# Optimization experiments

Hardware: AMD Instinct MI355X
Metric: run time of the kernel (lower is better)

## Reference

```python
import jax, jax.numpy as jnp
import numpy as np

V, EMB, ENC, DEC = 50000, 256, 512, 512
E2 = ENC * 2            # bidirectional encoder output dim = 1024
B, S1, S2 = 128, 200, 200
NEG = -1e10


def _bahdanau(hidden, enc_out, mask, W, b, v):
    # hidden [B,DEC], enc_out [S,B,E2], mask [B,S] -> weights [B,S]
    S = enc_out.shape[0]
    h = jnp.broadcast_to(hidden[None], (S,) + hidden.shape)          # [S,B,DEC]
    energy = jnp.tanh(jnp.concatenate([h, enc_out], axis=-1) @ W + b)  # [S,B,DEC]
    scores = energy @ v                                              # [S,B]
    scores = jnp.where(mask.T == 0, NEG, scores)
    return jax.nn.softmax(scores, axis=0).T                          # [B,S]


def setup_inputs() -> dict:
    key = jax.random.key(0)
    ks = jax.random.split(key, 20)
    f = lambda k, shp, s=0.05: jax.random.normal(k, shp, dtype=jnp.float32) * s
    inp = {
        "input": jax.random.randint(ks[0], (B,), 0, V),
        "hidden": f(ks[1], (B, DEC), 1.0),
        "src1": jax.random.randint(ks[2], (S1, B), 0, V),
        "encoder_outputs1": f(ks[3], (S1, B, E2), 1.0),
        "mask1": jnp.ones((B, S1), dtype=jnp.int32),
        "triple_mask": jnp.ones((B, S1), dtype=jnp.int32),
        "encoder_outputs2": f(ks[4], (S2, B, E2), 1.0),
        "mask2": jnp.ones((B, S2), dtype=jnp.int32),
        # parameters
        "embedding": f(ks[5], (V, EMB)),
        "attn_W": f(ks[6], (E2 + DEC, DEC)),
        "attn_b": jnp.zeros((DEC,), jnp.float32),
        "attn_v": f(ks[7], (DEC,)),
        "copy_W": f(ks[8], (E2 + DEC, DEC)),
        "copy_b": jnp.zeros((DEC,), jnp.float32),
        "copy_v": f(ks[9], (DEC,)),
        "gru_Wih": f(ks[10], (3 * DEC, E2 + EMB)),
        "gru_Whh": f(ks[11], (3 * DEC, DEC)),
        "gru_bih": jnp.zeros((3 * DEC,), jnp.float32),
        "gru_bhh": jnp.zeros((3 * DEC,), jnp.float32),
        "fc_W": f(ks[12], (V, E2 + DEC)),
        "fc_b": jnp.zeros((V,), jnp.float32),
        "gate_W": f(ks[13], (1, E2 + EMB)),
        "gate_b": jnp.zeros((1,), jnp.float32),
    }
    return inp


def reference(input, hidden, src1, encoder_outputs1, mask1, triple_mask,
              encoder_outputs2, mask2, embedding, attn_W, attn_b, attn_v,
              copy_W, copy_b, copy_v, gru_Wih, gru_Whh, gru_bih, gru_bhh,
              fc_W, fc_b, gate_W, gate_b):
    # embed current token (dropout = identity at eval)
    emb = embedding[input]                                           # [B,EMB]
    # joint attention over concatenated encoders
    enc = jnp.concatenate([encoder_outputs1, encoder_outputs2], axis=0)  # [S1+S2,B,E2]
    mask = jnp.concatenate([mask1, mask2], axis=1)                   # [B,S1+S2]
    a = _bahdanau(hidden, enc, mask, attn_W, attn_b, attn_v)         # [B,S1+S2]
    weighted = jnp.einsum('bs,sbe->be', a, enc)                      # [B,E2]
    # single-step GRU (PyTorch gate layout: r, z, n)
    x = jnp.concatenate([emb, weighted], axis=-1)                    # [B,E2+EMB]
    gx = x @ gru_Wih.T + gru_bih
    gh = hidden @ gru_Whh.T + gru_bhh
    xr, xz, xn = jnp.split(gx, 3, axis=-1)
    hr, hz, hn = jnp.split(gh, 3, axis=-1)
    r = jax.nn.sigmoid(xr + hr)
    z = jax.nn.sigmoid(xz + hz)
    n = jnp.tanh(xn + r * hn)
    h_new = (1.0 - z) * n + z * hidden                               # [B,DEC]
    # generation distribution
    state = jnp.concatenate([h_new, weighted], axis=1)               # [B,DEC+E2]
    vocab_dist = jax.nn.softmax(state @ fc_W.T + fc_b, axis=-1)      # [B,V]
    # copy gate + copy attention over encoder 1 only
    p_gen = jax.nn.sigmoid(jnp.concatenate([weighted, emb], axis=-1) @ gate_W.T + gate_b)  # [B,1]
    attn_dist = _bahdanau(h_new, encoder_outputs1, mask1 * triple_mask,
                          copy_W, copy_b, copy_v)                    # [B,S1]
    vd = p_gen * vocab_dist
    ad = (1.0 - p_gen) * attn_dist
    # scatter_add copy probabilities into vocab slots
    b_idx = jnp.arange(vd.shape[0])[:, None]                         # [B,1]
    final_dist = vd.at[b_idx, src1.T].add(ad)                        # [B,V]
    return final_dist, h_new
```

## Files before the change

kernel.cpp:

```cpp
#include <hip/hip_runtime.h>
#include <math.h>

#define BB   128
#define DECD 512
#define E2D  1024
#define EMBD 256
#define S1D  200
#define S2D  200
#define SJD  400
#define VV   50000
#define NEGV (-1e10f)
#define JY   800

typedef unsigned short u16;
typedef __bf16 bf16x8 __attribute__((ext_vector_type(8)));
typedef float f32x4 __attribute__((ext_vector_type(4)));
typedef u16 u16x8 __attribute__((ext_vector_type(8)));

__device__ __forceinline__ u16 f2bf(float x) {
  unsigned u = __float_as_uint(x);
  unsigned r = (u + 0x7fffu + ((u >> 16) & 1u)) >> 16;
  return (u16)r;
}
__device__ __forceinline__ float bf2f(u16 h) {
  return __uint_as_float(((unsigned)h) << 16);
}
__device__ __forceinline__ u16x8 cvt8h(float4 a, float4 b) {
  bf16x8 r;
  r[0] = (__bf16)a.x; r[1] = (__bf16)a.y; r[2] = (__bf16)a.z; r[3] = (__bf16)a.w;
  r[4] = (__bf16)b.x; r[5] = (__bf16)b.y; r[6] = (__bf16)b.z; r[7] = (__bf16)b.w;
  return *reinterpret_cast<u16x8*>(&r);
}

typedef const __attribute__((address_space(1))) void* gas_t;
typedef __attribute__((address_space(3))) void* las_t;
__device__ __forceinline__ void async_copy16(const u16* g, u16* l) {
  __builtin_amdgcn_global_load_lds((gas_t)g, (las_t)l, 16, 0, 0);
}

__global__ __launch_bounds__(256) void k_prep(
    const float* __restrict__ Wa, const float* __restrict__ Wc,
    u16* __restrict__ Wta, u16* __restrict__ Wtc,
    const float* __restrict__ hidden, u16* __restrict__ hid_bf,
    const float* __restrict__ attn_b, float* __restrict__ hWa,
    const int* __restrict__ inp, const float* __restrict__ table,
    u16* __restrict__ x_bf) {
  int blk = blockIdx.x, tid = threadIdx.x;
  if (blk < 1024) {
    __shared__ float t[32][33];
    int z = blk >> 9, rem = blk & 511;
    int bk = rem & 31, bn = rem >> 5;
    const float* W = z ? Wc : Wa;
    u16* Wt = z ? Wtc : Wta;
    int tx = tid & 31, ty = tid >> 5;
    #pragma unroll
    for (int r = 0; r < 4; ++r) {
      int k = bk * 32 + ty + r * 8;
      t[ty + r * 8][tx] = W[(size_t)(512 + k) * 512 + bn * 32 + tx];
    }
    __syncthreads();
    #pragma unroll
    for (int r = 0; r < 4; ++r) {
      int n = bn * 32 + ty + r * 8;
      Wt[(size_t)n * 1024 + bk * 32 + tx] = f2bf(t[tx][ty + r * 8]);
    }
  } else if (blk < 1056) {
    int i = (blk - 1024) * 256 + tid;
    const float4 f0 = *(const float4*)(hidden + (size_t)i * 8);
    const float4 f1 = *(const float4*)(hidden + (size_t)i * 8 + 4);
    *(u16x8*)(hid_bf + (size_t)i * 8) = cvt8h(f0, f1);
  } else if (blk < 1312) {
    int idx = blk - 1056;
    int b = idx >> 1;
    int d = (idx & 1) * 256 + tid;
    const float* hr = hidden + (size_t)b * DECD;
    float acc = attn_b[d];
    #pragma unroll 8
    for (int k = 0; k < DECD; ++k) acc += hr[k] * Wa[(size_t)k * DECD + d];
    hWa[(size_t)b * DECD + d] = acc;
  } else {
    int b = blk - 1312;
    x_bf[(size_t)b * 1280 + tid] = f2bf(table[(size_t)inp[b] * EMBD + tid]);
  }
}

__global__ __launch_bounds__(256) void gemm_energy_jc(
    const float* __restrict__ enc1, const float* __restrict__ enc2,
    const u16* __restrict__ BtA, const u16* __restrict__ BtC,
    const float* __restrict__ hW, const float* __restrict__ v,
    float* __restrict__ partJ, float* __restrict__ preC) {
  __shared__ u16 As[2][64 * 32];
  __shared__ u16 Bs[256 * 32];
  __shared__ float sbuf[64][2];
  int tid = threadIdx.x;
  int wid = tid >> 6, lane = tid & 63;
  int wr = wid >> 1, wc = wid & 1;
  int bn = blockIdx.x;
  int jy = blockIdx.y;
  int joint = (jy < JY);
  size_t m0 = joint ? (size_t)jy * 64 : (size_t)(jy - JY) * 64;
  int bhalf = (jy & 1) * 64;
  int n0 = bn * 256;

  int rA = tid >> 2, cslot = tid & 3;
  int lAoff = rA * 32 + ((cslot ^ ((rA >> 1) & 3)) * 8);
  const float* base;
  if (joint)
    base = (m0 < (size_t)S1D * BB) ? (enc1 + m0 * E2D)
                                   : (enc2 + (m0 - (size_t)S1D * BB) * E2D);
  else
    base = enc1 + m0 * E2D;
  const float* gA_f = base + (size_t)rA * E2D + cslot * 8;

  const u16* Bt = joint ? BtA : BtC;
  const u16* gB[4];
  #pragma unroll
  for (int i = 0; i < 4; ++i) {
    int rn = i * 64 + wid * 16 + (lane >> 2);
    int c = (lane & 3) ^ ((rn >> 1) & 3);
    gB[i] = Bt + (size_t)(n0 + rn) * E2D + c * 8;
  }

  int q = lane >> 4, cl = lane & 15;
  int aoff[2], boff[8];
  #pragma unroll
  for (int mi = 0; mi < 2; ++mi) {
    int row = wr * 32 + mi * 16 + cl;
    aoff[mi] = row * 64 + ((q ^ ((row >> 1) & 3)) * 16);
  }
  #pragma unroll
  for (int nj = 0; nj < 8; ++nj) {
    int rn = wc * 128 + nj * 16 + cl;
    boff[nj] = rn * 64 + ((q ^ ((rn >> 1) & 3)) * 16);
  }

  f32x4 acc[2][8];
  #pragma unroll
  for (int mi = 0; mi < 2; ++mi)
    #pragma unroll
    for (int nj = 0; nj < 8; ++nj) {
      f32x4 z = {0.f, 0.f, 0.f, 0.f};
      acc[mi][nj] = z;
    }

  float4 a0 = *(const float4*)(gA_f);
  float4 a1 = *(const float4*)(gA_f + 4);
  *(u16x8*)(&As[0][lAoff]) = cvt8h(a0, a1);
  a0 = *(const float4*)(gA_f + 32);
  a1 = *(const float4*)(gA_f + 36);

  for (int t = 0; t < 32; ++t) {
    int cur = t & 1, nxt = cur ^ 1;
    int k0 = t * 32, k1 = k0 + 32;
    #pragma unroll
    for (int i = 0; i < 4; ++i) async_copy16(gB[i] + k0, &Bs[2048 * i + wid * 512]);
    if (t < 31) {
      *(u16x8*)(&As[nxt][lAoff]) = cvt8h(a0, a1);
      if (t < 30) {
        a0 = *(const float4*)(gA_f + k1 + 32);
        a1 = *(const float4*)(gA_f + k1 + 36);
      }
    }
    __syncthreads();
    bf16x8 af[2];
    #pragma unroll
    for (int mi = 0; mi < 2; ++mi)
      af[mi] = *(const bf16x8*)((const char*)As[cur] + aoff[mi]);
    #pragma unroll
    for (int nj = 0; nj < 8; ++nj) {
      bf16x8 bg = *(const bf16x8*)((const char*)Bs + boff[nj]);
      acc[0][nj] = __builtin_amdgcn_mfma_f32_16x16x32_bf16(af[0], bg, acc[0][nj], 0, 0, 0);
      acc[1][nj] = __builtin_amdgcn_mfma_f32_16x16x32_bf16(af[1], bg, acc[1][nj], 0, 0, 0);
    }
    __syncthreads();
  }

  if (joint) {
    #pragma unroll
    for (int mi = 0; mi < 2; ++mi) {
      #pragma unroll
      for (int j = 0; j < 4; ++j) {
        int m = wr * 32 + mi * 16 + q * 4 + j;
        float s = 0.f;
        #pragma unroll
        for (int nj = 0; nj < 8; ++nj) {
          int d = n0 + wc * 128 + nj * 16 + cl;
          s += tanhf(acc[mi][nj][j] + hW[(size_t)(bhalf + m) * DECD + d]) * v[d];
        }
        s += __shfl_xor(s, 1, 64);
        s += __shfl_xor(s, 2, 64);
        s += __shfl_xor(s, 4, 64);
        s += __shfl_xor(s, 8, 64);
        if (cl == 0) sbuf[m][wc] = s;
      }
    }
    __syncthreads();
    if (tid < 64)
      partJ[(size_t)bn * 51200 + m0 + tid] = sbuf[tid][0] + sbuf[tid][1];
  } else {
    #pragma unroll
    for (int mi = 0; mi < 2; ++mi) {
      #pragma unroll
      for (int nj = 0; nj < 8; ++nj) {
        int d = n0 + wc * 128 + nj * 16 + cl;
        #pragma unroll
        for (int j = 0; j < 4; ++j) {
          int m = wr * 32 + mi * 16 + q * 4 + j;
          preC[(m0 + m) * (size_t)DECD + d] = acc[mi][nj][j];
        }
      }
    }
  }
}

__global__ __launch_bounds__(256) void k_copy_epi(const float* __restrict__ preC,
    const float* __restrict__ hWc, const float* __restrict__ v,
    float* __restrict__ scC) {
  int r = blockIdx.x * 4 + (threadIdx.x >> 6);
  int lane = threadIdx.x & 63;
  int b = r & 127, s = r >> 7;
  const float* pr = preC + (size_t)r * DECD + lane * 8;
  const float* hr = hWc + (size_t)b * DECD + lane * 8;
  const float* vr = v + lane * 8;
  float4 p0 = *(const float4*)(pr),     p1 = *(const float4*)(pr + 4);
  float4 h0 = *(const float4*)(hr),     h1 = *(const float4*)(hr + 4);
  float4 v0 = *(const float4*)(vr),     v1 = *(const float4*)(vr + 4);
  float acc = tanhf(p0.x + h0.x) * v0.x + tanhf(p0.y + h0.y) * v0.y
            + tanhf(p0.z + h0.z) * v0.z + tanhf(p0.w + h0.w) * v0.w
            + tanhf(p1.x + h1.x) * v1.x + tanhf(p1.y + h1.y) * v1.y
            + tanhf(p1.z + h1.z) * v1.z + tanhf(p1.w + h1.w) * v1.w;
  #pragma unroll
  for (int off = 32; off > 0; off >>= 1) acc += __shfl_xor(acc, off, 64);
  if (lane == 0) scC[(size_t)b * S1D + s] = acc;
}

__global__ __launch_bounds__(256) void k_wpart_sm(const float* __restrict__ part,
    const float* __restrict__ enc1, const float* __restrict__ enc2,
    const int* __restrict__ m1, const int* __restrict__ m2,
    float* __restrict__ wp) {
  int b = blockIdx.x, tid = threadIdx.x;
  int e2 = blockIdx.y * 256 + tid;
  int scn = blockIdx.z;
  __shared__ float sm[4];
  __shared__ float ws[100];
  int s0 = tid, s2 = tid + 256;
  float a0, a1 = -INFINITY;
  {
    int msk = (s0 < S1D) ? m1[b * S1D + s0] : m2[b * S2D + (s0 - S1D)];
    int m = s0 * 128 + b;
    a0 = msk ? (part[m] + part[51200 + m]) : NEGV;
  }
  if (s2 < SJD) {
    int msk = (s2 < S1D) ? m1[b * S1D + s2] : m2[b * S2D + (s2 - S1D)];
    int m = s2 * 128 + b;
    a1 = msk ? (part[m] + part[51200 + m]) : NEGV;
  }
  float vmax = fmaxf(a0, a1);
  #pragma unroll
  for (int off = 32; off > 0; off >>= 1) vmax = fmaxf(vmax, __shfl_down(vmax, off, 64));
  int lane = tid & 63, wid = tid >> 6;
  if (lane == 0) sm[wid] = vmax;
  __syncthreads();
  vmax = fmaxf(fmaxf(sm[0], sm[1]), fmaxf(sm[2], sm[3]));
  __syncthreads();
  float lsum = expf(a0 - vmax);
  if (s2 < SJD) lsum += expf(a1 - vmax);
  #pragma unroll
  for (int off = 32; off > 0; off >>= 1) lsum += __shfl_down(lsum, off, 64);
  if (lane == 0) sm[wid] = lsum;
  __syncthreads();
  float inv = 1.0f / (sm[0] + sm[1] + sm[2] + sm[3]);
  if (tid < 100) {
    int s = scn * 100 + tid;
    int msk = (s < S1D) ? m1[b * S1D + s] : m2[b * S2D + (s - S1D)];
    int m = s * 128 + b;
    float av = msk ? (part[m] + part[51200 + m]) : NEGV;
    ws[tid] = expf(av - vmax) * inv;
  }
  __syncthreads();
  float acc0 = 0.f, acc1 = 0.f;
  #pragma unroll 4
  for (int i = 0; i < 100; ++i) {
    int s = scn * 100 + i;
    const float* ep = (s < S1D) ? (enc1 + ((size_t)s * BB + b) * E2D)
                                : (enc2 + ((size_t)(s - S1D) * BB + b) * E2D);
    float2 u = *(const float2*)(ep + e2 * 2);
    float w = ws[i];
    acc0 += w * u.x;
    acc1 += w * u.y;
  }
  float* dst = wp + ((size_t)scn * BB + b) * E2D + e2 * 2;
  dst[0] = acc0;
  dst[1] = acc1;
}

__global__ __launch_bounds__(256) void k_wsum_x(const float* __restrict__ wp,
    float* __restrict__ wgt, u16* __restrict__ x) {
  int i = blockIdx.x * 256 + threadIdx.x;
  const int NN = BB * E2D;
  float s = wp[i] + wp[NN + i] + wp[2 * NN + i] + wp[3 * NN + i];
  wgt[i] = s;
  int b = i >> 10, e = i & 1023;
  x[(size_t)b * 1280 + EMBD + e] = f2bf(s);
}

__device__ __forceinline__ void fc2_body(
    const u16* __restrict__ A, const float* __restrict__ Bf,
    const float* __restrict__ bias, float* __restrict__ C,
    int N, int K, int n0) {
  __shared__ u16 As[2][128 * 32];
  __shared__ u16 Bs[2][128 * 32];
  int tid = threadIdx.x;
  int wid = tid >> 6, lane = tid & 63;
  int wr = wid >> 2, wc = wid & 3;

  int rowa = wid * 16 + (lane >> 2);
  int ca = (lane & 3) ^ ((rowa >> 1) & 3);
  const u16* gA = A + (size_t)rowa * K + ca * 8;

  int rB = tid >> 2, cB = tid & 3;
  int gnB = n0 + rB; if (gnB >= N) gnB = N - 1;
  const float* gB = Bf + (size_t)gnB * K + cB * 8;
  int lBoff = rB * 32 + ((cB ^ ((rB >> 1) & 3)) * 8);

  int q = lane >> 4, cl = lane & 15;
  int aoff[4], boff[2];
  #pragma unroll
  for (int mi = 0; mi < 4; ++mi) {
    int row = wr * 64 + mi * 16 + cl;
    aoff[mi] = row * 64 + ((q ^ ((row >> 1) & 3)) * 16);
  }
  #pragma unroll
  for (int nj = 0; nj < 2; ++nj) {
    int rn = wc * 32 + nj * 16 + cl;
    boff[nj] = rn * 64 + ((q ^ ((rn >> 1) & 3)) * 16);
  }

  f32x4 acc[4][2];
  #pragma unroll
  for (int mi = 0; mi < 4; ++mi)
    #pragma unroll
    for (int nj = 0; nj < 2; ++nj) {
      f32x4 z = {0.f, 0.f, 0.f, 0.f};
      acc[mi][nj] = z;
    }

  for (int k0 = 0; k0 < K; k0 += 64) {
    float4 b00 = *(const float4*)(gB + k0);
    float4 b01 = *(const float4*)(gB + k0 + 4);
    float4 b10 = *(const float4*)(gB + k0 + 32);
    float4 b11 = *(const float4*)(gB + k0 + 36);
    *(u16x8*)(&Bs[0][lBoff]) = cvt8h(b00, b01);
    *(u16x8*)(&Bs[1][lBoff]) = cvt8h(b10, b11);
    async_copy16(gA + k0,      &As[0][wid * 512]);
    async_copy16(gA + k0 + 32, &As[1][wid * 512]);
    __syncthreads();
    #pragma unroll
    for (int h = 0; h < 2; ++h) {
      bf16x8 af[4], bg[2];
      #pragma unroll
      for (int mi = 0; mi < 4; ++mi) af[mi] = *(const bf16x8*)((const char*)As[h] + aoff[mi]);
      #pragma unroll
      for (int nj = 0; nj < 2; ++nj) bg[nj] = *(const bf16x8*)((const char*)Bs[h] + boff[nj]);
      #pragma unroll
      for (int mi = 0; mi < 4; ++mi)
        #pragma unroll
        for (int nj = 0; nj < 2; ++nj)
          acc[mi][nj] = __builtin_amdgcn_mfma_f32_16x16x32_bf16(af[mi], bg[nj], acc[mi][nj], 0, 0, 0);
    }
    __syncthreads();
  }

  #pragma unroll
  for (int mi = 0; mi < 4; ++mi) {
    #pragma unroll
    for (int nj = 0; nj < 2; ++nj) {
      int n = n0 + wc * 32 + nj * 16 + cl;
      if (n < N) {
        float bv = bias[n];
        #pragma unroll
        for (int j = 0; j < 4; ++j) {
          int m = wr * 64 + mi * 16 + q * 4 + j;
          C[(size_t)m * N + n] = acc[mi][nj][j] + bv;
        }
      }
    }
  }
}

__global__ __launch_bounds__(512) void gemm_gru(
    const u16* __restrict__ x_bf, const float* __restrict__ Wih,
    const float* __restrict__ bih, float* __restrict__ gx,
    const u16* __restrict__ h_bf, const float* __restrict__ Whh,
    const float* __restrict__ bhh, float* __restrict__ gh) {
  if (blockIdx.x < 12)
    fc2_body(x_bf, Wih, bih, gx, 1536, 1280, blockIdx.x * 128);
  else
    fc2_body(h_bf, Whh, bhh, gh, 1536, 512, (blockIdx.x - 12) * 128);
}

__global__ __launch_bounds__(512) void gemm_fc3(
    const u16* __restrict__ A, const float* __restrict__ Bf,
    const float* __restrict__ bias, float* __restrict__ C,
    int N, int K) {
  __shared__ u16 As[2][128 * 32];
  __shared__ u16 Bs[2][64 * 32];
  int tid = threadIdx.x;
  int wid = tid >> 6, lane = tid & 63;
  int wr = wid >> 2, wc = wid & 3;
  int n0 = blockIdx.x * 64;

  int rowa = wid * 16 + (lane >> 2);
  int ca = (lane & 3) ^ ((rowa >> 1) & 3);
  const u16* gA = A + (size_t)rowa * K + ca * 8;

  int rB = tid >> 3, cB = tid & 7;
  int gnB = n0 + rB; if (gnB >= N) gnB = N - 1;
  const float* gB = Bf + (size_t)gnB * K + cB * 8;
  int hB = cB >> 2, s4 = cB & 3;
  int lBoff = rB * 32 + ((s4 ^ ((rB >> 1) & 3)) * 8);

  int q = lane >> 4, cl = lane & 15;
  int aoff[4], boff;
  #pragma unroll
  for (int mi = 0; mi < 4; ++mi) {
    int row = wr * 64 + mi * 16 + cl;
    aoff[mi] = row * 64 + ((q ^ ((row >> 1) & 3)) * 16);
  }
  {
    int rn = wc * 16 + cl;
    boff = rn * 64 + ((q ^ ((rn >> 1) & 3)) * 16);
  }

  f32x4 acc[4];
  #pragma unroll
  for (int mi = 0; mi < 4; ++mi) {
    f32x4 z = {0.f, 0.f, 0.f, 0.f};
    acc[mi] = z;
  }

  float4 b0 = *(const float4*)(gB);
  float4 b1 = *(const float4*)(gB + 4);

  for (int k0 = 0; k0 < K; k0 += 64) {
    *(u16x8*)(&Bs[hB][lBoff]) = cvt8h(b0, b1);
    async_copy16(gA + k0,      &As[0][wid * 512]);
    async_copy16(gA + k0 + 32, &As[1][wid * 512]);
    __syncthreads();
    if (k0 + 64 < K) {
      b0 = *(const float4*)(gB + k0 + 64);
      b1 = *(const float4*)(gB + k0 + 68);
    }
    #pragma unroll
    for (int h = 0; h < 2; ++h) {
      bf16x8 af[4];
      #pragma unroll
      for (int mi = 0; mi < 4; ++mi) af[mi] = *(const bf16x8*)((const char*)As[h] + aoff[mi]);
      bf16x8 bg = *(const bf16x8*)((const char*)Bs[h] + boff);
      #pragma unroll
      for (int mi = 0; mi < 4; ++mi)
        acc[mi] = __builtin_amdgcn_mfma_f32_16x16x32_bf16(af[mi], bg, acc[mi], 0, 0, 0);
    }
    __syncthreads();
  }

  int n = n0 + wc * 16 + cl;
  if (n < N) {
    float bv = bias[n];
    #pragma unroll
    for (int mi = 0; mi < 4; ++mi)
      #pragma unroll
      for (int j = 0; j < 4; ++j) {
        int m = wr * 64 + mi * 16 + q * 4 + j;
        C[(size_t)m * N + n] = acc[mi][j] + bv;
      }
  }
}

__global__ __launch_bounds__(256) void k_gru_concat(const float* __restrict__ gx,
    const float* __restrict__ gh, const float* __restrict__ hidden,
    const float* __restrict__ wgt, float* __restrict__ hnew,
    u16* __restrict__ st) {
  int b = blockIdx.x, tid = threadIdx.x;
  #pragma unroll
  for (int qq = 0; qq < 2; ++qq) {
    int d = tid + qq * 256;
    size_t o = (size_t)b * 1536;
    float xr = gx[o + d],        hr = gh[o + d];
    float xz = gx[o + 512 + d],  hz = gh[o + 512 + d];
    float xn = gx[o + 1024 + d], hn = gh[o + 1024 + d];
    float r = 1.f / (1.f + expf(-(xr + hr)));
    float z = 1.f / (1.f + expf(-(xz + hz)));
    float n = tanhf(xn + r * hn);
    float hv = (1.f - z) * n + z * hidden[(size_t)b * DECD + d];
    hnew[(size_t)b * DECD + d] = hv;
    st[(size_t)b * 1536 + d] = f2bf(hv);
  }
  #pragma unroll
  for (int qq = 0; qq < 4; ++qq) {
    int e = tid + qq * 256;
    st[(size_t)b * 1536 + DECD + e] = f2bf(wgt[(size_t)b * E2D + e]);
  }
}

__global__ __launch_bounds__(256) void k_pgen_partial(const float* __restrict__ wgt,
    const int* __restrict__ inp, const float* __restrict__ table,
    const float* __restrict__ gW, const float* __restrict__ gb,
    float* __restrict__ pg,
    const float* __restrict__ hnew, const float* __restrict__ copy_W,
    const float* __restrict__ copy_b, float* __restrict__ hWc) {
  int tid = threadIdx.x;
  if (blockIdx.x < 128) {
    int b = blockIdx.x;
    __shared__ float sm[4];
    float s = 0.f;
    for (int k = tid; k < E2D + EMBD; k += 256)
      s += gW[k] * ((k < E2D) ? wgt[(size_t)b * E2D + k]
                              : table[(size_t)inp[b] * EMBD + k - E2D]);
    #pragma unroll
    for (int off = 32; off > 0; off >>= 1) s += __shfl_down(s, off, 64);
    int lane = tid & 63, wid = tid >> 6;
    if (lane == 0) sm[wid] = s;
    __syncthreads();
    if (tid == 0) {
      float t = sm[0] + sm[1] + sm[2] + sm[3] + gb[0];
      pg[b] = 1.f / (1.f + expf(-t));
    }
  } else {
    int idx = blockIdx.x - 128;
    int b = idx >> 1;
    int d = (idx & 1) * 256 + tid;
    const float* hr = hnew + (size_t)b * DECD;
    float acc = copy_b[d];
    #pragma unroll 8
    for (int k = 0; k < DECD; ++k) acc += hr[k] * copy_W[(size_t)k * DECD + d];
    hWc[(size_t)b * DECD + d] = acc;
  }
}

__global__ __launch_bounds__(256) void k_vocab_sc2(float* __restrict__ dist,
    const float* __restrict__ pg, const float* __restrict__ scC,
    const int* __restrict__ m1, const int* __restrict__ tr,
    const int* __restrict__ src1) {
  int b = blockIdx.x, tid = threadIdx.x;
  float* row = dist + (size_t)b * VV;
  __shared__ float sm[4];
  int lane = tid & 63, wid = tid >> 6;
  float m = -INFINITY;
  for (int i = tid; i < VV; i += 256) m = fmaxf(m, row[i]);
  #pragma unroll
  for (int off = 32; off > 0; off >>= 1) m = fmaxf(m, __shfl_down(m, off, 64));
  if (lane == 0) sm[wid] = m;
  __syncthreads();
  m = fmaxf(fmaxf(sm[0], sm[1]), fmaxf(sm[2], sm[3]));
  __syncthreads();
  float s = 0.f;
  for (int i = tid; i < VV; i += 256) s += expf(row[i] - m);
  #pragma unroll
  for (int off = 32; off > 0; off >>= 1) s += __shfl_down(s, off, 64);
  if (lane == 0) sm[wid] = s;
  __syncthreads();
  s = sm[0] + sm[1] + sm[2] + sm[3];
  float pgb = pg[b];
  float scale = pgb / s;
  for (int i = tid; i < VV; i += 256) row[i] = expf(row[i] - m) * scale;
  __syncthreads();
  float c0 = -INFINITY;
  if (tid < S1D) {
    int msk = m1[b * S1D + tid] * tr[b * S1D + tid];
    c0 = msk ? scC[(size_t)b * S1D + tid] : NEGV;
  }
  float cmax = c0;
  #pragma unroll
  for (int off = 32; off > 0; off >>= 1) cmax = fmaxf(cmax, __shfl_down(cmax, off, 64));
  if (lane == 0) sm[wid] = cmax;
  __syncthreads();
  cmax = fmaxf(fmaxf(sm[0], sm[1]), fmaxf(sm[2], sm[3]));
  __syncthreads();
  float csum = (tid < S1D) ? expf(c0 - cmax) : 0.f;
  #pragma unroll
  for (int off = 32; off > 0; off >>= 1) csum += __shfl_down(csum, off, 64);
  if (lane == 0) sm[wid] = csum;
  __syncthreads();
  float cinv = 1.0f / (sm[0] + sm[1] + sm[2] + sm[3]);
  if (tid < S1D) {
    float val = (1.f - pgb) * expf(c0 - cmax) * cinv;
    int tok = src1[(size_t)tid * BB + b];
    atomicAdd(&row[tok], val);
  }
}

extern "C" void kernel_launch(void* const* d_in, const int* in_sizes, int n_in,
                              void* d_out, int out_size, void* d_ws, size_t ws_size,
                              hipStream_t stream) {
  (void)in_sizes; (void)n_in; (void)out_size; (void)ws_size;
  const int*   input  = (const int*)d_in[0];
  const float* hidden = (const float*)d_in[1];
  const int*   src1   = (const int*)d_in[2];
  const float* enc1   = (const float*)d_in[3];
  const int*   mask1  = (const int*)d_in[4];
  const int*   triple = (const int*)d_in[5];
  const float* enc2   = (const float*)d_in[6];
  const int*   mask2  = (const int*)d_in[7];
  const float* embedding = (const float*)d_in[8];
  const float* attn_W = (const float*)d_in[9];
  const float* attn_b = (const float*)d_in[10];
  const float* attn_v = (const float*)d_in[11];
  const float* copy_W = (const float*)d_in[12];
  const float* copy_b = (const float*)d_in[13];
  const float* copy_v = (const float*)d_in[14];
  const float* gru_Wih = (const float*)d_in[15];
  const float* gru_Whh = (const float*)d_in[16];
  const float* gru_bih = (const float*)d_in[17];
  const float* gru_bhh = (const float*)d_in[18];
  const float* fc_W   = (const float*)d_in[19];
  const float* fc_b   = (const float*)d_in[20];
  const float* gate_W = (const float*)d_in[21];
  const float* gate_b = (const float*)d_in[22];

  char* w = (char*)d_ws;
  u16* Wt_a = (u16*)w;                w += (size_t)512 * 1024 * 2;
  u16* Wt_c = (u16*)w;                w += (size_t)512 * 1024 * 2;
  float* partJ = (float*)w;           w += (size_t)2 * 51200 * 4;
  float* preC = (float*)w;            w += (size_t)25600 * 512 * 4;
  float* hWa  = (float*)w;            w += (size_t)BB * DECD * 4;
  float* hWc  = (float*)w;            w += (size_t)BB * DECD * 4;
  float* scC  = (float*)w;            w += (size_t)BB * S1D * 4;
  float* wgt  = (float*)w;            w += (size_t)BB * E2D * 4;
  float* wpart = (float*)w;           w += (size_t)4 * BB * E2D * 4;
  u16*   x_bf = (u16*)w;              w += (size_t)BB * 1280 * 2;
  u16*   hid_bf = (u16*)w;            w += (size_t)BB * DECD * 2;
  float* gx   = (float*)w;            w += (size_t)BB * 1536 * 4;
  float* gh   = (float*)w;            w += (size_t)BB * 1536 * 4;
  u16*   st_bf = (u16*)w;             w += (size_t)BB * 1536 * 2;
  float* pg   = (float*)w;            w += 512;

  float* out  = (float*)d_out;
  float* hnew = out + (size_t)BB * VV;

  k_prep<<<1440, 256, 0, stream>>>(attn_W, copy_W, Wt_a, Wt_c,
                                   hidden, hid_bf, attn_b, hWa,
                                   input, embedding, x_bf);

  gemm_energy_jc<<<dim3(2, JY + 400), 256, 0, stream>>>(
      enc1, enc2, Wt_a, Wt_c, hWa, attn_v, partJ, preC);

  k_wpart_sm<<<dim3(BB, 2, 4), 256, 0, stream>>>(partJ, enc1, enc2, mask1, mask2, wpart);
  k_wsum_x<<<512, 256, 0, stream>>>(wpart, wgt, x_bf);

  gemm_gru<<<24, 512, 0, stream>>>(x_bf, gru_Wih, gru_bih, gx,
                                   hid_bf, gru_Whh, gru_bhh, gh);
  k_gru_concat<<<BB, 256, 0, stream>>>(gx, gh, hidden, wgt, hnew, st_bf);

  gemm_fc3<<<(VV + 63) / 64, 512, 0, stream>>>(st_bf, fc_W, fc_b, out, VV, 1536);

  k_pgen_partial<<<384, 256, 0, stream>>>(wgt, input, embedding, gate_W, gate_b, pg,
                                          hnew, copy_W, copy_b, hWc);
  k_copy_epi<<<25600 / 4, 256, 0, stream>>>(preC, hWc, copy_v, scC);

  k_vocab_sc2<<<BB, 256, 0, stream>>>(out, pg, scC, mask1, triple, src1);
}
```

Baseline: 576.6 us.

## Fuse p_gen, copy-hidden projection and copy scores into the fc GEMM launch

New measurement: 565.5 us. No clear change (-1.9%).

```diff
diff --git a/kernel.cpp b/kernel.cpp
--- a/kernel.cpp
+++ b/kernel.cpp
@@ -213,27 +213,6 @@
   }
 }
 
-__global__ __launch_bounds__(256) void k_copy_epi(const float* __restrict__ preC,
-    const float* __restrict__ hWc, const float* __restrict__ v,
-    float* __restrict__ scC) {
-  int r = blockIdx.x * 4 + (threadIdx.x >> 6);
-  int lane = threadIdx.x & 63;
-  int b = r & 127, s = r >> 7;
-  const float* pr = preC + (size_t)r * DECD + lane * 8;
-  const float* hr = hWc + (size_t)b * DECD + lane * 8;
-  const float* vr = v + lane * 8;
-  float4 p0 = *(const float4*)(pr),     p1 = *(const float4*)(pr + 4);
-  float4 h0 = *(const float4*)(hr),     h1 = *(const float4*)(hr + 4);
-  float4 v0 = *(const float4*)(vr),     v1 = *(const float4*)(vr + 4);
-  float acc = tanhf(p0.x + h0.x) * v0.x + tanhf(p0.y + h0.y) * v0.y
-            + tanhf(p0.z + h0.z) * v0.z + tanhf(p0.w + h0.w) * v0.w
-            + tanhf(p1.x + h1.x) * v1.x + tanhf(p1.y + h1.y) * v1.y
-            + tanhf(p1.z + h1.z) * v1.z + tanhf(p1.w + h1.w) * v1.w;
-  #pragma unroll
-  for (int off = 32; off > 0; off >>= 1) acc += __shfl_xor(acc, off, 64);
-  if (lane == 0) scC[(size_t)b * S1D + s] = acc;
-}
-
 __global__ __launch_bounds__(256) void k_wpart_sm(const float* __restrict__ part,
     const float* __restrict__ enc1, const float* __restrict__ enc2,
     const int* __restrict__ m1, const int* __restrict__ m2,
@@ -399,81 +378,137 @@
     fc2_body(h_bf, Whh, bhh, gh, 1536, 512, (blockIdx.x - 12) * 128);
 }
 
-__global__ __launch_bounds__(512) void gemm_fc3(
+__global__ __launch_bounds__(512) void gemm_fc3c(
     const u16* __restrict__ A, const float* __restrict__ Bf,
-    const float* __restrict__ bias, float* __restrict__ C,
-    int N, int K) {
-  __shared__ u16 As[2][128 * 32];
-  __shared__ u16 Bs[2][64 * 32];
+    const float* __restrict__ bias, float* __restrict__ C, int N, int K,
+    const float* __restrict__ wgt, const int* __restrict__ inp,
+    const float* __restrict__ table, const float* __restrict__ gW,
+    const float* __restrict__ gb, float* __restrict__ pg,
+    const float* __restrict__ hnew, const float* __restrict__ copy_W,
+    const float* __restrict__ copy_b, const float* __restrict__ copy_v,
+    const float* __restrict__ preC, float* __restrict__ scC) {
+  __shared__ u16 smem[12288];
   int tid = threadIdx.x;
-  int wid = tid >> 6, lane = tid & 63;
-  int wr = wid >> 2, wc = wid & 3;
-  int n0 = blockIdx.x * 64;
-
-  int rowa = wid * 16 + (lane >> 2);
-  int ca = (lane & 3) ^ ((rowa >> 1) & 3);
-  const u16* gA = A + (size_t)rowa * K + ca * 8;
-
-  int rB = tid >> 3, cB = tid & 7;
-  int gnB = n0 + rB; if (gnB >= N) gnB = N - 1;
-  const float* gB = Bf + (size_t)gnB * K + cB * 8;
-  int hB = cB >> 2, s4 = cB & 3;
-  int lBoff = rB * 32 + ((s4 ^ ((rB >> 1) & 3)) * 8);
-
-  int q = lane >> 4, cl = lane & 15;
-  int aoff[4], boff;
-  #pragma unroll
-  for (int mi = 0; mi < 4; ++mi) {
-    int row = wr * 64 + mi * 16 + cl;
-    aoff[mi] = row * 64 + ((q ^ ((row >> 1) & 3)) * 16);
-  }
-  {
-    int rn = wc * 16 + cl;
-    boff = rn * 64 + ((q ^ ((rn >> 1) & 3)) * 16);
-  }
-
-  f32x4 acc[4];
-  #pragma unroll
-  for (int mi = 0; mi < 4; ++mi) {
-    f32x4 z = {0.f, 0.f, 0.f, 0.f};
-    acc[mi] = z;
-  }
-
-  float4 b0 = *(const float4*)(gB);
-  float4 b1 = *(const float4*)(gB + 4);
-
-  for (int k0 = 0; k0 < K; k0 += 64) {
-    *(u16x8*)(&Bs[hB][lBoff]) = cvt8h(b0, b1);
-    async_copy16(gA + k0,      &As[0][wid * 512]);
-    async_copy16(gA + k0 + 32, &As[1][wid * 512]);
-    __syncthreads();
-    if (k0 + 64 < K) {
-      b0 = *(const float4*)(gB + k0 + 64);
-      b1 = *(const float4*)(gB + k0 + 68);
-    }
-    #pragma unroll
-    for (int h = 0; h < 2; ++h) {
-      bf16x8 af[4];
-      #pragma unroll
-      for (int mi = 0; mi < 4; ++mi) af[mi] = *(const bf16x8*)((const char*)As[h] + aoff[mi]);
-      bf16x8 bg = *(const bf16x8*)((const char*)Bs[h] + boff);
+  if (blockIdx.x < 782) {
+    u16* As0 = smem;            u16* As1 = smem + 4096;
+    u16* Bs0 = smem + 8192;     u16* Bs1 = smem + 10240;
+    u16* AsH[2] = {As0, As1};
+    u16* BsH[2] = {Bs0, Bs1};
+    int wid = tid >> 6, lane = tid & 63;
+    int wr = wid >> 2, wc = wid & 3;
+    int n0 = blockIdx.x * 64;
+
+    int rowa = wid * 16 + (lane >> 2);
+    int ca = (lane & 3) ^ ((rowa >> 1) & 3);
+    const u16* gA = A + (size_t)rowa * K + ca * 8;
+
+    int rB = tid >> 3, cB = tid & 7;
+    int gnB = n0 + rB; if (gnB >= N) gnB = N - 1;
+    const float* gB = Bf + (size_t)gnB * K + cB * 8;
+    int hB = cB >> 2, s4 = cB & 3;
+    int lBoff = rB * 32 + ((s4 ^ ((rB >> 1) & 3)) * 8);
+
+    int q = lane >> 4, cl = lane & 15;
+    int aoff[4], boff;
+    #pragma unroll
+    for (int mi = 0; mi < 4; ++mi) {
+      int row = wr * 64 + mi * 16 + cl;
+      aoff[mi] = row * 64 + ((q ^ ((row >> 1) & 3)) * 16);
+    }
+    {
+      int rn = wc * 16 + cl;
+      boff = rn * 64 + ((q ^ ((rn >> 1) & 3)) * 16);
+    }
+
+    f32x4 acc[4];
+    #pragma unroll
+    for (int mi = 0; mi < 4; ++mi) {
+      f32x4 z = {0.f, 0.f, 0.f, 0.f};
+      acc[mi] = z;
+    }
+
+    float4 b0 = *(const float4*)(gB);
+    float4 b1 = *(const float4*)(gB + 4);
+
+    for (int k0 = 0; k0 < K; k0 += 64) {
+      *(u16x8*)(&BsH[hB][lBoff]) = cvt8h(b0, b1);
+      async_copy16(gA + k0,      &As0[wid * 512]);
+      async_copy16(gA + k0 + 32, &As1[wid * 512]);
+      __syncthreads();
+      if (k0 + 64 < K) {
+        b0 = *(const float4*)(gB + k0 + 64);
+        b1 = *(const float4*)(gB + k0 + 68);
+      }
+      #pragma unroll
+      for (int h = 0; h < 2; ++h) {
+        bf16x8 af[4];
+        #pragma unroll
+        for (int mi = 0; mi < 4; ++mi) af[mi] = *(const bf16x8*)((const char*)AsH[h] + aoff[mi]);
+        bf16x8 bg = *(const bf16x8*)((const char*)BsH[h] + boff);
+        #pragma unroll
+        for (int mi = 0; mi < 4; ++mi)
+          acc[mi] = __builtin_amdgcn_mfma_f32_16x16x32_bf16(af[mi], bg, acc[mi], 0, 0, 0);
+      }
+      __syncthreads();
+    }
+
+    int n = n0 + wc * 16 + cl;
+    if (n < N) {
+      float bv = bias[n];
       #pragma unroll
       for (int mi = 0; mi < 4; ++mi)
-        acc[mi] = __builtin_amdgcn_mfma_f32_16x16x32_bf16(af[mi], bg, acc[mi], 0, 0, 0);
-    }
-    __syncthreads();
-  }
-
-  int n = n0 + wc * 16 + cl;
-  if (n < N) {
-    float bv = bias[n];
-    #pragma unroll
-    for (int mi = 0; mi < 4; ++mi)
-      #pragma unroll
-      for (int j = 0; j < 4; ++j) {
-        int m = wr * 64 + mi * 16 + q * 4 + j;
-        C[(size_t)m * N + n] = acc[mi][j] + bv;
-      }
+        #pragma unroll
+        for (int j = 0; j < 4; ++j) {
+          int m = wr * 64 + mi * 16 + q * 4 + j;
+          C[(size_t)m * N + n] = acc[mi][j] + bv;
+        }
+    }
+  } else if (blockIdx.x < 910) {
+    int b = blockIdx.x - 782;
+    float* sm = (float*)smem;
+    float s = 0.f;
+    for (int k = tid; k < E2D + EMBD; k += 512)
+      s += gW[k] * ((k < E2D) ? wgt[(size_t)b * E2D + k]
+                              : table[(size_t)inp[b] * EMBD + k - E2D]);
+    #pragma unroll
+    for (int off = 32; off > 0; off >>= 1) s += __shfl_down(s, off, 64);
+    int lane = tid & 63, wid = tid >> 6;
+    if (lane == 0) sm[wid] = s;
+    __syncthreads();
+    if (tid == 0) {
+      float t = sm[0] + sm[1] + sm[2] + sm[3] + sm[4] + sm[5] + sm[6] + sm[7] + gb[0];
+      pg[b] = 1.f / (1.f + expf(-t));
+    }
+  } else {
+    int b = blockIdx.x - 910;
+    float* hn  = (float*)smem;
+    float* hwc = (float*)smem + 512;
+    hn[tid] = hnew[(size_t)b * DECD + tid];
+    __syncthreads();
+    {
+      float acc = copy_b[tid];
+      #pragma unroll 8
+      for (int k = 0; k < DECD; ++k) acc += hn[k] * copy_W[(size_t)k * DECD + tid];
+      hwc[tid] = acc;
+    }
+    __syncthreads();
+    int wid = tid >> 6, lane = tid & 63;
+    float4 h0 = *(const float4*)(hwc + lane * 8);
+    float4 h1 = *(const float4*)(hwc + lane * 8 + 4);
+    float4 v0 = *(const float4*)(copy_v + lane * 8);
+    float4 v1 = *(const float4*)(copy_v + lane * 8 + 4);
+    for (int s = wid; s < S1D; s += 8) {
+      const float* pr = preC + ((size_t)s * 128 + b) * DECD + lane * 8;
+      float4 p0 = *(const float4*)(pr);
+      float4 p1 = *(const float4*)(pr + 4);
+      float e = tanhf(p0.x + h0.x) * v0.x + tanhf(p0.y + h0.y) * v0.y
+              + tanhf(p0.z + h0.z) * v0.z + tanhf(p0.w + h0.w) * v0.w
+              + tanhf(p1.x + h1.x) * v1.x + tanhf(p1.y + h1.y) * v1.y
+              + tanhf(p1.z + h1.z) * v1.z + tanhf(p1.w + h1.w) * v1.w;
+      #pragma unroll
+      for (int off = 32; off > 0; off >>= 1) e += __shfl_xor(e, off, 64);
+      if (lane == 0) scC[(size_t)b * S1D + s] = e;
+    }
   }
 }
 
@@ -500,41 +535,6 @@
   for (int qq = 0; qq < 4; ++qq) {
     int e = tid + qq * 256;
     st[(size_t)b * 1536 + DECD + e] = f2bf(wgt[(size_t)b * E2D + e]);
-  }
-}
-
-__global__ __launch_bounds__(256) void k_pgen_partial(const float* __restrict__ wgt,
-    const int* __restrict__ inp, const float* __restrict__ table,
-    const float* __restrict__ gW, const float* __restrict__ gb,
-    float* __restrict__ pg,
-    const float* __restrict__ hnew, const float* __restrict__ copy_W,
-    const float* __restrict__ copy_b, float* __restrict__ hWc) {
-  int tid = threadIdx.x;
-  if (blockIdx.x < 128) {
-    int b = blockIdx.x;
-    __shared__ float sm[4];
-    float s = 0.f;
-    for (int k = tid; k < E2D + EMBD; k += 256)
-      s += gW[k] * ((k < E2D) ? wgt[(size_t)b * E2D + k]
-                              : table[(size_t)inp[b] * EMBD + k - E2D]);
-    #pragma unroll
-    for (int off = 32; off > 0; off >>= 1) s += __shfl_down(s, off, 64);
-    int lane = tid & 63, wid = tid >> 6;
-    if (lane == 0) sm[wid] = s;
-    __syncthreads();
-    if (tid == 0) {
-      float t = sm[0] + sm[1] + sm[2] + sm[3] + gb[0];
-      pg[b] = 1.f / (1.f + expf(-t));
-    }
-  } else {
-    int idx = blockIdx.x - 128;
-    int b = idx >> 1;
-    int d = (idx & 1) * 256 + tid;
-    const float* hr = hnew + (size_t)b * DECD;
-    float acc = copy_b[d];
-    #pragma unroll 8
-    for (int k = 0; k < DECD; ++k) acc += hr[k] * copy_W[(size_t)k * DECD + d];
-    hWc[(size_t)b * DECD + d] = acc;
   }
 }
 
@@ -624,7 +624,6 @@
   float* partJ = (float*)w;           w += (size_t)2 * 51200 * 4;
   float* preC = (float*)w;            w += (size_t)25600 * 512 * 4;
   float* hWa  = (float*)w;            w += (size_t)BB * DECD * 4;
-  float* hWc  = (float*)w;            w += (size_t)BB * DECD * 4;
   float* scC  = (float*)w;            w += (size_t)BB * S1D * 4;
   float* wgt  = (float*)w;            w += (size_t)BB * E2D * 4;
   float* wpart = (float*)w;           w += (size_t)4 * BB * E2D * 4;
@@ -652,11 +651,10 @@
                                    hid_bf, gru_Whh, gru_bhh, gh);
   k_gru_concat<<<BB, 256, 0, stream>>>(gx, gh, hidden, wgt, hnew, st_bf);
 
-  gemm_fc3<<<(VV + 63) / 64, 512, 0, stream>>>(st_bf, fc_W, fc_b, out, VV, 1536);
-
-  k_pgen_partial<<<384, 256, 0, stream>>>(wgt, input, embedding, gate_W, gate_b, pg,
-                                          hnew, copy_W, copy_b, hWc);
-  k_copy_epi<<<25600 / 4, 256, 0, stream>>>(preC, hWc, copy_v, scC);
+  gemm_fc3c<<<782 + 128 + 128, 512, 0, stream>>>(
+      st_bf, fc_W, fc_b, out, VV, 1536,
+      wgt, input, embedding, gate_W, gate_b, pg,
+      hnew, copy_W, copy_b, copy_v, preC, scC);
 
   k_vocab_sc2<<<BB, 256, 0, stream>>>(out, pg, scC, mask1, triple, src1);
 }
```
